# Optimization experiments

Measured on AMD Instinct MI355X. Metric: run time of the kernel, lower is better.

The kernel has to match this reference:

```python
import jax, jax.numpy as jnp
import numpy as np
import math

B, L, LC = 2, 2048, 2048
D_MODEL, D_CROSS, D_HEAD = 1024, 1024, 64
N_HEADS = D_MODEL // D_HEAD
D6 = D_HEAD // 6  # freq bands per spatial axis (k-diffusion AxialRoPE, 3 axes)
EPS = 1e-6


def rope_freqs():
    n = N_HEADS * D6
    f = jnp.exp(jnp.linspace(math.log(math.pi), math.log(10.0 * math.pi), n + 1)[:-1])
    return f.reshape(D6, N_HEADS).T  # [nh, d6]


def rope_theta(pos):
    # pos: [b, l, 3] -> theta: [b, nh, l, 3*d6]
    f = rope_freqs()
    th = jnp.concatenate([pos[..., None, a:a + 1] * f for a in range(3)], axis=-1)  # [b,l,nh,3*d6]
    return jnp.moveaxis(th, -2, -3)


def apply_rotary(x, theta):
    d = theta.shape[-1]
    x1, x2, x3 = x[..., :d], x[..., d:2 * d], x[..., 2 * d:]
    c, s = jnp.cos(theta), jnp.sin(theta)
    return jnp.concatenate([x1 * c - x2 * s, x2 * c + x1 * s, x3], axis=-1)


def rms_norm(x, scale, eps=EPS):
    ms = jnp.mean(x * x, axis=-1, keepdims=True)
    return x * (scale * jax.lax.rsqrt(ms + eps))


def cosine_scale(q, k, scale, eps=EPS):
    s = jnp.sqrt(scale)[:, None, None]  # [nh,1,1]
    qn = q * (s * jax.lax.rsqrt(jnp.sum(q * q, axis=-1, keepdims=True) + eps))
    kn = k * (s * jax.lax.rsqrt(jnp.sum(k * k, axis=-1, keepdims=True) + eps))
    return qn, kn


def setup_inputs():
    key = jax.random.key(0)
    ks = jax.random.split(key, 8)
    return {
        "x": jax.random.normal(ks[0], (B, L, D_MODEL), jnp.float32),
        "pos": jax.random.uniform(ks[1], (B, L, 3), jnp.float32),
        "x_cross": jax.random.normal(ks[2], (B, LC, D_CROSS), jnp.float32),
        "pos_cross": jax.random.uniform(ks[3], (B, LC, 3), jnp.float32),
        "norm_scale": jnp.ones((D_MODEL,), jnp.float32),
        "norm_cross_scale": jnp.ones((D_CROSS,), jnp.float32),
        "q_w": jax.random.normal(ks[4], (D_MODEL, D_MODEL), jnp.float32) * 0.02,
        "kv_w": jax.random.normal(ks[5], (2 * D_MODEL, D_CROSS), jnp.float32) * 0.02,
        "head_scale": jnp.full((N_HEADS,), 10.0, jnp.float32),
        "out_w": jax.random.normal(ks[6], (D_MODEL, D_MODEL), jnp.float32) * 0.02,
    }


def reference(x, pos, x_cross, pos_cross, norm_scale, norm_cross_scale, q_w, kv_w, head_scale, out_w):
    skip = x
    xn = rms_norm(x, norm_scale)
    xc = rms_norm(x_cross, norm_cross_scale)
    q = xn @ q_w.T                       # [b,l,d]
    kv = xc @ kv_w.T                     # [b,lc,2d]
    b, l, _ = q.shape
    lc = kv.shape[1]
    q = q.reshape(b, l, N_HEADS, D_HEAD).transpose(0, 2, 1, 3)          # [b,nh,l,e]
    kv = kv.reshape(b, lc, 2, N_HEADS, D_HEAD)                          # (t nh e) factorization
    k = kv[:, :, 0].transpose(0, 2, 1, 3)
    v = kv[:, :, 1].transpose(0, 2, 1, 3)
    q, k = cosine_scale(q, k, head_scale)
    q = apply_rotary(q, rope_theta(pos))
    k = apply_rotary(k, rope_theta(pos_cross))
    attn = jax.nn.softmax(jnp.einsum('bhqe,bhke->bhqk', q, k), axis=-1)  # scale=1.0 (cosine-sim pre-scaled)
    o = jnp.einsum('bhqk,bhke->bhqe', attn, v)
    o = o.transpose(0, 2, 1, 3).reshape(b, l, D_MODEL)
    return o @ out_w.T + skip
```

## Files before the change

### kernel.cpp

```cpp
#include <hip/hip_runtime.h>

typedef __bf16 bf16_t;
typedef __bf16 bf16x4 __attribute__((ext_vector_type(4)));
typedef __bf16 bf16x8 __attribute__((ext_vector_type(8)));
typedef float f32x4 __attribute__((ext_vector_type(4)));
typedef short s16x4 __attribute__((ext_vector_type(4)));

#define B_DIM 2
#define L_DIM 2048
#define LC_DIM 2048
#define DM 1024
#define NH 16
#define DH 64
#define MB (1u << 20)
#define LOG2E 1.44269504088896f

__device__ __forceinline__ bool probe_is_f32(const unsigned* probe) {
  return probe[0] == 0x3F800000u;
}

__device__ __forceinline__ void async16(const bf16_t* g, bf16_t* l) {
  __builtin_amdgcn_global_load_lds((const __attribute__((address_space(1))) void*)g,
                                   (__attribute__((address_space(3))) void*)l, 16, 0, 0);
}

#if __has_builtin(__builtin_amdgcn_mfma_f32_16x16x16bf16_1k)
#define HAVE_K16 1
__device__ __forceinline__ f32x4 mfma16(bf16x4 a, bf16x4 b, f32x4 c) {
  union { bf16x4 h; s16x4 s; } ua, ub;
  ua.h = a; ub.h = b;
  return __builtin_amdgcn_mfma_f32_16x16x16bf16_1k(ua.s, ub.s, c, 0, 0, 0);
}
#else
#define HAVE_K16 0
#endif

__device__ __forceinline__ void conv_b(const void* src, bf16_t* dst, int i, bool f32) {
  bf16x4 w;
  if (f32) {
    f32x4 v = *(const f32x4*)((const float*)src + i);
    w[0] = (bf16_t)v[0]; w[1] = (bf16_t)v[1]; w[2] = (bf16_t)v[2]; w[3] = (bf16_t)v[3];
  } else {
    w = *(const bf16x4*)((const bf16_t*)src + i);
  }
  *(bf16x4*)(dst + i) = w;
}
__device__ __forceinline__ void conv_f(const void* src, float* dst, int i, int n, bool f32) {
  if (i >= n) return;
  f32x4 v;
  if (f32) {
    v = *(const f32x4*)((const float*)src + i);
  } else {
    bf16x4 w = *(const bf16x4*)((const bf16_t*)src + i);
    v[0] = (float)w[0]; v[1] = (float)w[1]; v[2] = (float)w[2]; v[3] = (float)w[3];
  }
  *(f32x4*)(dst + i) = v;
}

__global__ __launch_bounds__(256) void front_k(
    const void* x, const void* xc, const void* qw, const void* kvw, const void* ow,
    const void* pos, const void* posc, const void* ns, const void* ncs, const void* hs,
    bf16_t* xn, bf16_t* xcn, bf16_t* cqw, bf16_t* ckvw, bf16_t* cow,
    float* fpos, float* fposc, float* fns, float* fncs, float* fhs,
    const unsigned* probe) {
  const bool f32 = probe_is_f32(probe);
  const int tid = threadIdx.x;
  if (blockIdx.x < 2 * B_DIM * L_DIM) {
    const bool isB = blockIdx.x >= B_DIM * L_DIM;
    const int row = isB ? blockIdx.x - B_DIM * L_DIM : blockIdx.x;
    const void* src = isB ? xc : x;
    const void* scr = isB ? ncs : ns;
    bf16_t* out = isB ? xcn : xn;
    float f0, f1, f2, f3, s0, s1, s2, s3;
    if (f32) {
      f32x4 v = *((const f32x4*)((const float*)src + (size_t)row * DM) + tid);
      f0 = v[0]; f1 = v[1]; f2 = v[2]; f3 = v[3];
      f32x4 sv = *((const f32x4*)scr + tid);
      s0 = sv[0]; s1 = sv[1]; s2 = sv[2]; s3 = sv[3];
    } else {
      bf16x4 v = *((const bf16x4*)((const bf16_t*)src + (size_t)row * DM) + tid);
      f0 = (float)v[0]; f1 = (float)v[1]; f2 = (float)v[2]; f3 = (float)v[3];
      bf16x4 sv = *((const bf16x4*)scr + tid);
      s0 = (float)sv[0]; s1 = (float)sv[1]; s2 = (float)sv[2]; s3 = (float)sv[3];
    }
    float ss = f0 * f0 + f1 * f1 + f2 * f2 + f3 * f3;
#pragma unroll
    for (int m = 1; m < 64; m <<= 1) ss += __shfl_xor(ss, m, 64);
    __shared__ float red[4];
    const int wave = tid >> 6, lane = tid & 63;
    if (lane == 0) red[wave] = ss;
    __syncthreads();
    float ms = (red[0] + red[1] + red[2] + red[3]) * (1.0f / DM);
    float r = rsqrtf(ms + 1e-6f);
    bf16x4 w;
    w[0] = (bf16_t)(f0 * r * s0);
    w[1] = (bf16_t)(f1 * r * s1);
    w[2] = (bf16_t)(f2 * r * s2);
    w[3] = (bf16_t)(f3 * r * s3);
    *(bf16x4*)(out + (size_t)row * DM + tid * 4) = w;
    return;
  }
  const int blk = blockIdx.x - 2 * B_DIM * L_DIM;
  const int e4 = tid * 4;
  if (blk < 1024)       conv_b(qw,  cqw,  blk * 1024 + e4, f32);
  else if (blk < 3072)  conv_b(kvw, ckvw, (blk - 1024) * 1024 + e4, f32);
  else if (blk < 4096)  conv_b(ow,  cow,  (blk - 3072) * 1024 + e4, f32);
  else if (blk < 4108)  conv_f(pos,  fpos,  (blk - 4096) * 1024 + e4, 12288, f32);
  else if (blk < 4120)  conv_f(posc, fposc, (blk - 4108) * 1024 + e4, 12288, f32);
  else if (blk == 4120) conv_f(ns,  fns,  e4, 1024, f32);
  else if (blk == 4121) conv_f(ncs, fncs, e4, 1024, f32);
  else                  conv_f(hs,  fhs,  e4, 16, f32);
}

__global__ __launch_bounds__(256) void gemm_qkv_k(const bf16_t* __restrict__ xn,
                                                  const bf16_t* __restrict__ xcn,
                                                  const bf16_t* __restrict__ qw,
                                                  const bf16_t* __restrict__ kvw,
                                                  bf16_t* __restrict__ qb,
                                                  bf16_t* __restrict__ kvK,
                                                  bf16_t* __restrict__ Vp) {
  __shared__ bf16_t Asm[128 * 32];
  __shared__ bf16_t Wsm[128 * 32];
  const int tid = threadIdx.x;
  const int wave = tid >> 6, lane = tid & 63;
  const int quad = lane >> 4, tc = lane & 15;
  const int wr = wave >> 1, wc = wave & 1;
  const bool isq = blockIdx.y < 8;
  const bf16_t* A = isq ? xn : xcn;
  const bf16_t* W = isq ? qw : kvw;
  const int n0 = (isq ? blockIdx.y : (blockIdx.y - 8)) * 128;
  const int m0 = blockIdx.x * 128;
  const int K = 1024;

  const int srow = wave * 16 + (lane >> 2);
  const int scol = (lane & 3) * 8;
  const bf16_t* ag = A + (size_t)(m0 + srow) * K + scol;
  const bf16_t* wg = W + (size_t)(n0 + srow) * K + scol;
  bf16_t* al0 = &Asm[(wave * 16) * 32];
  bf16_t* al1 = &Asm[(64 + wave * 16) * 32];
  bf16_t* wl0 = &Wsm[(wave * 16) * 32];
  bf16_t* wl1 = &Wsm[(64 + wave * 16) * 32];

  f32x4 acc[4][4] = {};

  for (int k0 = 0; k0 < K; k0 += 32) {
    async16(ag + k0, al0);
    async16(ag + k0 + (size_t)64 * K, al1);
    async16(wg + k0, wl0);
    async16(wg + k0 + (size_t)64 * K, wl1);
    __syncthreads();
    bf16x8 af[4], wf[4];
#pragma unroll
    for (int i = 0; i < 4; ++i)
      af[i] = *(const bf16x8*)&Asm[(wr * 64 + i * 16 + tc) * 32 + quad * 8];
#pragma unroll
    for (int j = 0; j < 4; ++j)
      wf[j] = *(const bf16x8*)&Wsm[(wc * 64 + j * 16 + tc) * 32 + quad * 8];
#pragma unroll
    for (int i = 0; i < 4; ++i)
#pragma unroll
      for (int j = 0; j < 4; ++j)
        acc[i][j] = __builtin_amdgcn_mfma_f32_16x16x32_bf16(af[i], wf[j], acc[i][j], 0, 0, 0);
    __syncthreads();
  }

  if (isq || n0 < DM) {
    bf16_t* C = isq ? qb : kvK;
#pragma unroll
    for (int i = 0; i < 4; ++i) {
      const size_t row = (size_t)m0 + wr * 64 + i * 16 + quad * 4;
#pragma unroll
      for (int j = 0; j < 4; ++j) {
        const int col = n0 + wc * 64 + j * 16 + tc;
#pragma unroll
        for (int r = 0; r < 4; ++r)
          C[(row + r) * DM + col] = (bf16_t)acc[i][j][r];
      }
    }
  } else {
#pragma unroll
    for (int i = 0; i < 4; ++i) {
      const int row = m0 + wr * 64 + i * 16 + quad * 4;
      const int b = row >> 11, kc = row & (LC_DIM - 1);
#pragma unroll
      for (int j = 0; j < 4; ++j) {
        const int hd = n0 - DM + wc * 64 + j * 16 + tc;
        const int h = hd >> 6, d = hd & 63;
        bf16x4 pk;
        pk[0] = (bf16_t)acc[i][j][0];
        pk[1] = (bf16_t)acc[i][j][1];
        pk[2] = (bf16_t)acc[i][j][2];
        pk[3] = (bf16_t)acc[i][j][3];
        *(bf16x4*)(Vp + (((size_t)(b * NH + h) * (LC_DIM / 4) + (kc >> 2)) * DH + d) * 4) = pk;
      }
    }
  }
}

__global__ __launch_bounds__(256) void prep_k(bf16_t* __restrict__ q,
                                              const bf16_t* __restrict__ kvK,
                                              bf16_t* __restrict__ Kp,
                                              const float* __restrict__ pos,
                                              const float* __restrict__ pos_cross,
                                              const float* __restrict__ head_scale) {
  const int gw = (blockIdx.x * blockDim.x + threadIdx.x) >> 6;
  const int lane = threadIdx.x & 63;
  const int per = B_DIM * L_DIM * NH;
  const bool is_k = gw >= per;
  const int id = is_k ? gw - per : gw;
  const int h = id & 15;
  const int row = id >> 4;
  const bf16_t* src = (is_k ? kvK : q) + (size_t)row * DM + h * DH;
  const float* pp = (is_k ? pos_cross : pos) + (size_t)row * 3;

  float val = (float)src[lane];
  float ss = val * val;
#pragma unroll
  for (int m = 1; m < 64; m <<= 1) ss += __shfl_xor(ss, m, 64);
  float sc = sqrtf(head_scale[h]) * rsqrtf(ss + 1e-6f);
  if (!is_k) sc *= LOG2E;
  float vn = val * sc;

  const int j = lane;
  const int tj = j < 30 ? j : (j < 60 ? j - 30 : 0);
  const int a = tj >= 20 ? 2 : (tj >= 10 ? 1 : 0);
  const int jj = tj - a * 10;
  float p = pp[a];
  float freq = 3.14159265358979f * expf((float)(jj * 16 + h) * 0.014391156831f);
  float th = p * freq;
  float cth = cosf(th), sth = sinf(th);
  const int partner = j < 30 ? j + 30 : (j < 60 ? j - 30 : j);
  float vp = __shfl(vn, partner, 64);
  float outv;
  if (j < 30)       outv = vn * cth - vp * sth;
  else if (j < 60)  outv = vn * cth + vp * sth;
  else              outv = vn;

  if (is_k) {
    const int b = row >> 11, l = row & (LC_DIM - 1);
    Kp[(((size_t)b * NH + h) * LC_DIM + l) * DH + lane] = (bf16_t)outv;
  } else {
    q[(size_t)row * DM + h * DH + lane] = (bf16_t)outv;
  }
}

__global__ __launch_bounds__(64, 4) void flash6_k(const bf16_t* __restrict__ q,
                                                  const bf16_t* __restrict__ Kp,
                                                  const bf16_t* __restrict__ Vp,
                                                  bf16_t* __restrict__ Op,
                                                  float* __restrict__ lp) {
  const int lane = threadIdx.x;
  const int quad = lane >> 4, tc = lane & 15;
  const int bh = blockIdx.y, b = bh >> 4;
  const int z = blockIdx.z;
  const int q0 = blockIdx.x * 32;

  bf16x8 qf[2][2];
#pragma unroll
  for (int jj = 0; jj < 2; ++jj)
#pragma unroll
    for (int hf = 0; hf < 2; ++hf)
      qf[jj][hf] = *(const bf16x8*)(q + (size_t)(b * L_DIM + q0 + jj * 16 + tc) * DM +
                                    (bh & 15) * DH + hf * 32 + quad * 8);

  f32x4 accO[2][4] = {};
  const bf16_t* kg = Kp + (size_t)bh * LC_DIM * DH;
  const bf16_t* vp = Vp + (size_t)bh * (LC_DIM / 4) * DH * 4;

#if HAVE_K16
  f32x4 accL[2] = {};
  bf16x4 ones;
  ones[0] = (bf16_t)1.0f; ones[1] = (bf16_t)1.0f;
  ones[2] = (bf16_t)1.0f; ones[3] = (bf16_t)1.0f;
#else
  __shared__ bf16_t Psm[32 * 64];
  float lsum[2] = {0.f, 0.f};
  const int sw = tc & 7;
#endif

#pragma unroll 1
  for (int kc0 = z * 1024; kc0 < z * 1024 + 1024; kc0 += 64) {
    bf16x8 kfr[4][2];
#pragma unroll
    for (int mt = 0; mt < 4; ++mt)
#pragma unroll
      for (int hf = 0; hf < 2; ++hf)
        kfr[mt][hf] = *(const bf16x8*)(kg + (size_t)(kc0 + mt * 16 + tc) * DH +
                                       hf * 32 + quad * 8);

#if HAVE_K16
    bf16x4 vf[4][4];
#pragma unroll
    for (int mt = 0; mt < 4; ++mt)
#pragma unroll
      for (int dt = 0; dt < 4; ++dt)
        vf[mt][dt] = *(const bf16x4*)(vp + ((size_t)((kc0 >> 2) + mt * 4 + quad) * DH +
                                            dt * 16 + tc) * 4);

#pragma unroll
    for (int jj = 0; jj < 2; ++jj) {
      f32x4 s[4];
#pragma unroll
      for (int mt = 0; mt < 4; ++mt) {
        f32x4 zf = {0.f, 0.f, 0.f, 0.f};
        zf = __builtin_amdgcn_mfma_f32_16x16x32_bf16(kfr[mt][0], qf[jj][0], zf, 0, 0, 0);
        zf = __builtin_amdgcn_mfma_f32_16x16x32_bf16(kfr[mt][1], qf[jj][1], zf, 0, 0, 0);
        s[mt] = zf;
      }
      bf16x4 p[4];
#pragma unroll
      for (int mt = 0; mt < 4; ++mt) {
        p[mt][0] = (bf16_t)__builtin_amdgcn_exp2f(s[mt][0]);
        p[mt][1] = (bf16_t)__builtin_amdgcn_exp2f(s[mt][1]);
        p[mt][2] = (bf16_t)__builtin_amdgcn_exp2f(s[mt][2]);
        p[mt][3] = (bf16_t)__builtin_amdgcn_exp2f(s[mt][3]);
      }
#pragma unroll
      for (int mt = 0; mt < 4; ++mt) {
        accL[jj] = mfma16(p[mt], ones, accL[jj]);
#pragma unroll
        for (int dt = 0; dt < 4; ++dt)
          accO[jj][dt] = mfma16(p[mt], vf[mt][dt], accO[jj][dt]);
      }
    }
#else
#pragma unroll
    for (int jj = 0; jj < 2; ++jj) {
      f32x4 s[4];
#pragma unroll
      for (int mt = 0; mt < 4; ++mt) {
        f32x4 zf = {0.f, 0.f, 0.f, 0.f};
        zf = __builtin_amdgcn_mfma_f32_16x16x32_bf16(kfr[mt][0], qf[jj][0], zf, 0, 0, 0);
        zf = __builtin_amdgcn_mfma_f32_16x16x32_bf16(kfr[mt][1], qf[jj][1], zf, 0, 0, 0);
        s[mt] = zf;
      }
#pragma unroll
      for (int mt = 0; mt < 4; ++mt) {
        float p0 = __builtin_amdgcn_exp2f(s[mt][0]);
        float p1 = __builtin_amdgcn_exp2f(s[mt][1]);
        float p2 = __builtin_amdgcn_exp2f(s[mt][2]);
        float p3 = __builtin_amdgcn_exp2f(s[mt][3]);
        lsum[jj] += (p0 + p1) + (p2 + p3);
        bf16x4 pk;
        pk[0] = (bf16_t)p0; pk[1] = (bf16_t)p1; pk[2] = (bf16_t)p2; pk[3] = (bf16_t)p3;
        const int phys = (mt * 2 + (quad >> 1)) ^ sw;
        *(bf16x4*)&Psm[(jj * 16 + tc) * 64 + phys * 8 + (quad & 1) * 4] = pk;
      }
    }
#pragma unroll
    for (int kb = 0; kb < 2; ++kb) {
      bf16x8 vfull[4];
#pragma unroll
      for (int dt = 0; dt < 4; ++dt) {
        const size_t k4 = (size_t)((kc0 + kb * 32) >> 2) + quad * 2;
        bf16x4 lo = *(const bf16x4*)(vp + (k4 * DH + dt * 16 + tc) * 4);
        bf16x4 hi = *(const bf16x4*)(vp + ((k4 + 1) * DH + dt * 16 + tc) * 4);
#pragma unroll
        for (int e = 0; e < 4; ++e) { vfull[dt][e] = lo[e]; vfull[dt][4 + e] = hi[e]; }
      }
#pragma unroll
      for (int jp = 0; jp < 2; ++jp) {
        bf16x8 pf = *(const bf16x8*)&Psm[(jp * 16 + tc) * 64 + ((kb * 4 + quad) ^ sw) * 8];
#pragma unroll
        for (int dt = 0; dt < 4; ++dt)
          accO[jp][dt] = __builtin_amdgcn_mfma_f32_16x16x32_bf16(pf, vfull[dt], accO[jp][dt], 0, 0, 0);
      }
    }
#endif
  }

  bf16_t* Ob = Op + (size_t)(z * 32 + bh) * L_DIM * DH;
  float* lb = lp + (size_t)(z * 32 + bh) * L_DIM;
#if HAVE_K16
#pragma unroll
  for (int jj = 0; jj < 2; ++jj) {
    if (tc == 0) {
#pragma unroll
      for (int r = 0; r < 4; ++r) lb[q0 + jj * 16 + quad * 4 + r] = accL[jj][r];
    }
#pragma unroll
    for (int r = 0; r < 4; ++r) {
      const size_t qg = q0 + jj * 16 + quad * 4 + r;
#pragma unroll
      for (int dt = 0; dt < 4; ++dt)
        Ob[qg * DH + dt * 16 + tc] = (bf16_t)accO[jj][dt][r];
    }
  }
#else
#pragma unroll
  for (int jj = 0; jj < 2; ++jj) {
    lsum[jj] += __shfl_xor(lsum[jj], 16, 64);
    lsum[jj] += __shfl_xor(lsum[jj], 32, 64);
  }
#pragma unroll
  for (int jj = 0; jj < 2; ++jj) {
    if (quad == 0) lb[q0 + jj * 16 + tc] = lsum[jj];
#pragma unroll
    for (int r = 0; r < 4; ++r) {
      const size_t qg = q0 + jj * 16 + quad * 4 + r;
#pragma unroll
      for (int dt = 0; dt < 4; ++dt)
        Ob[qg * DH + dt * 16 + tc] = (bf16_t)accO[jj][dt][r];
    }
  }
#endif
}

__global__ __launch_bounds__(256) void combine_k(const bf16_t* __restrict__ Op,
                                                 const float* __restrict__ lp,
                                                 bf16_t* __restrict__ ob) {
  const size_t t = (size_t)blockIdx.x * 256 + threadIdx.x;
  const int bh = (int)(t >> 15);
  const int rem = (int)(t & 32767);
  const int l = rem >> 4, d4 = (rem & 15) * 4;
  const size_t base = ((size_t)bh * L_DIM + l) * DH + d4;
  const size_t zoff = (size_t)32 * L_DIM * DH;
  bf16x4 a0 = *(const bf16x4*)(Op + base);
  bf16x4 a1 = *(const bf16x4*)(Op + zoff + base);
  const float linv = 1.f / (lp[(size_t)bh * L_DIM + l] + lp[(size_t)32 * L_DIM + bh * L_DIM + l]);
  bf16x4 w;
#pragma unroll
  for (int e = 0; e < 4; ++e) w[e] = (bf16_t)(((float)a0[e] + (float)a1[e]) * linv);
  const int b = bh >> 4, h = bh & 15;
  *(bf16x4*)(ob + ((size_t)(b * L_DIM + l)) * DM + h * DH + d4) = w;
}

__global__ __launch_bounds__(256) void gemm_out_k(const bf16_t* __restrict__ A,
                                                  const bf16_t* __restrict__ W,
                                                  const void* __restrict__ skip_raw,
                                                  void* __restrict__ out,
                                                  const unsigned* __restrict__ probe) {
  __shared__ bf16_t Asm[64 * 32];
  __shared__ bf16_t Wsm[128 * 32];
  const int tid = threadIdx.x;
  const int wave = tid >> 6, lane = tid & 63;
  const int quad = lane >> 4, tc = lane & 15;
  const int wr = wave >> 1, wc = wave & 1;
  const int m0 = blockIdx.x * 64, n0 = blockIdx.y * 128;
  const int K = 1024, N = 1024;

  const int srow = wave * 16 + (lane >> 2);
  const int scol = (lane & 3) * 8;
  const bf16_t* ag = A + (size_t)(m0 + srow) * K + scol;
  const bf16_t* wg = W + (size_t)(n0 + srow) * K + scol;
  bf16_t* al = &Asm[(wave * 16) * 32];
  bf16_t* wl0 = &Wsm[(wave * 16) * 32];
  bf16_t* wl1 = &Wsm[(64 + wave * 16) * 32];

  f32x4 acc[2][4] = {};

  for (int k0 = 0; k0 < K; k0 += 32) {
    async16(ag + k0, al);
    async16(wg + k0, wl0);
    async16(wg + k0 + (size_t)64 * K, wl1);
    __syncthreads();
    bf16x8 af[2], wf[4];
#pragma unroll
    for (int i = 0; i < 2; ++i)
      af[i] = *(const bf16x8*)&Asm[(wr * 32 + i * 16 + tc) * 32 + quad * 8];
#pragma unroll
    for (int j = 0; j < 4; ++j)
      wf[j] = *(const bf16x8*)&Wsm[(wc * 64 + j * 16 + tc) * 32 + quad * 8];
#pragma unroll
    for (int i = 0; i < 2; ++i)
#pragma unroll
      for (int j = 0; j < 4; ++j)
        acc[i][j] = __builtin_amdgcn_mfma_f32_16x16x32_bf16(af[i], wf[j], acc[i][j], 0, 0, 0);
    __syncthreads();
  }

  const bool f32o = probe_is_f32(probe);
#pragma unroll
  for (int i = 0; i < 2; ++i) {
    const size_t row = (size_t)m0 + wr * 32 + i * 16 + quad * 4;
#pragma unroll
    for (int j = 0; j < 4; ++j) {
      const int col = n0 + wc * 64 + j * 16 + tc;
#pragma unroll
      for (int r = 0; r < 4; ++r) {
        const size_t idx = (row + r) * (size_t)N + col;
        float v = acc[i][j][r];
        if (f32o) {
          v += ((const float*)skip_raw)[idx];
          ((float*)out)[idx] = v;
        } else {
          v += (float)((const bf16_t*)skip_raw)[idx];
          ((bf16_t*)out)[idx] = (bf16_t)v;
        }
      }
    }
  }
}

extern "C" void kernel_launch(void* const* d_in, const int* in_sizes, int n_in,
                              void* d_out, int out_size, void* d_ws, size_t ws_size,
                              hipStream_t stream) {
  const unsigned* probe = (const unsigned*)d_in[4];
  char* ws = (char*)d_ws;

  bf16_t* cow  = (bf16_t*)(ws + 0 * MB);
  bf16_t* cqw  = (bf16_t*)(ws + 2 * MB);
  bf16_t* ckvw = (bf16_t*)(ws + 4 * MB);
  bf16_t* xn   = (bf16_t*)(ws + 8 * MB);
  bf16_t* xcn  = (bf16_t*)(ws + 16 * MB);
  bf16_t* Op   = (bf16_t*)(ws + 8 * MB);
  bf16_t* kvK  = (bf16_t*)(ws + 24 * MB);
  bf16_t* qb   = (bf16_t*)(ws + 32 * MB);
  bf16_t* Vp   = (bf16_t*)(ws + 40 * MB);
  bf16_t* Kp   = (bf16_t*)(ws + 48 * MB);
  bf16_t* ob   = (bf16_t*)(ws + 56 * MB);
  float* lp    = (float*)(ws + 64 * MB);
  float* fpos  = (float*)(ws + 65 * MB);
  float* fposc = (float*)(ws + 65 * MB + 64 * 1024);
  float* fns   = (float*)(ws + 65 * MB + 128 * 1024);
  float* fncs  = (float*)(ws + 65 * MB + 144 * 1024);
  float* fhs   = (float*)(ws + 65 * MB + 160 * 1024);

  front_k<<<2 * B_DIM * L_DIM + 4123, 256, 0, stream>>>(
      d_in[0], d_in[2], d_in[6], d_in[7], d_in[9], d_in[1], d_in[3], d_in[4],
      d_in[5], d_in[8], xn, xcn, cqw, ckvw, cow, fpos, fposc, fns, fncs, fhs, probe);
  gemm_qkv_k<<<dim3(32, 24), 256, 0, stream>>>(xn, xcn, cqw, ckvw, qb, kvK, Vp);
  prep_k<<<(2 * B_DIM * L_DIM * NH) / 4, 256, 0, stream>>>(qb, kvK, Kp, fpos, fposc, fhs);
  flash6_k<<<dim3(L_DIM / 32, B_DIM * NH, 2), 64, 0, stream>>>(qb, Kp, Vp, Op, lp);
  combine_k<<<4096, 256, 0, stream>>>(Op, lp, ob);
  gemm_out_k<<<dim3(64, 8), 256, 0, stream>>>(ob, cow, d_in[0], d_out, probe);
}
```

Before: 293.1 us.

## Double-buffer K/V register loads and double query rows per flash wave

The flash attention kernel now gives each 64-thread block 64 query rows instead of 32. This halves the number of blocks and doubles how often each loaded K/V tile is reused. In the MFMA path, K and V fragments are software-pipelined with two register buffers, so the next 64-key tile loads while the current one is being computed. The cost is much higher register pressure, with launch bounds lowered to 2 blocks per CU, and less parallelism across the grid.

```diff
diff --git a/kernel.cpp b/kernel.cpp
--- a/kernel.cpp
+++ b/kernel.cpp
@@ -244,7 +244,44 @@
   }
 }
 
-__global__ __launch_bounds__(64, 4) void flash6_k(const bf16_t* __restrict__ q,
+#define FLASH_LOAD(KB, VB, KC)                                                   \
+  {                                                                              \
+    _Pragma("unroll") for (int mt = 0; mt < 4; ++mt) {                           \
+      _Pragma("unroll") for (int hf = 0; hf < 2; ++hf)                           \
+        KB[mt][hf] = *(const bf16x8*)(kg + (size_t)((KC) + mt * 16 + tc) * DH +  \
+                                      hf * 32 + quad * 8);                       \
+      _Pragma("unroll") for (int dt = 0; dt < 4; ++dt)                           \
+        VB[mt][dt] = *(const bf16x4*)(vp + ((size_t)(((KC) >> 2) + mt * 4 + quad) * DH + \
+                                            dt * 16 + tc) * 4);                  \
+    }                                                                            \
+  }
+
+#define FLASH_COMPUTE(KB, VB)                                                    \
+  {                                                                              \
+    _Pragma("unroll") for (int jj = 0; jj < 4; ++jj) {                           \
+      f32x4 s[4];                                                                \
+      _Pragma("unroll") for (int mt = 0; mt < 4; ++mt) {                         \
+        f32x4 zf = {0.f, 0.f, 0.f, 0.f};                                         \
+        zf = __builtin_amdgcn_mfma_f32_16x16x32_bf16(KB[mt][0], qf[jj][0], zf, 0, 0, 0); \
+        zf = __builtin_amdgcn_mfma_f32_16x16x32_bf16(KB[mt][1], qf[jj][1], zf, 0, 0, 0); \
+        s[mt] = zf;                                                              \
+      }                                                                          \
+      bf16x4 p[4];                                                               \
+      _Pragma("unroll") for (int mt = 0; mt < 4; ++mt) {                         \
+        p[mt][0] = (bf16_t)__builtin_amdgcn_exp2f(s[mt][0]);                     \
+        p[mt][1] = (bf16_t)__builtin_amdgcn_exp2f(s[mt][1]);                     \
+        p[mt][2] = (bf16_t)__builtin_amdgcn_exp2f(s[mt][2]);                     \
+        p[mt][3] = (bf16_t)__builtin_amdgcn_exp2f(s[mt][3]);                     \
+      }                                                                          \
+      _Pragma("unroll") for (int mt = 0; mt < 4; ++mt) {                         \
+        accL[jj] = mfma16(p[mt], ones, accL[jj]);                                \
+        _Pragma("unroll") for (int dt = 0; dt < 4; ++dt)                         \
+          accO[jj][dt] = mfma16(p[mt], VB[mt][dt], accO[jj][dt]);                \
+      }                                                                          \
+    }                                                                            \
+  }
+
+__global__ __launch_bounds__(64, 2) void flash7_k(const bf16_t* __restrict__ q,
                                                   const bf16_t* __restrict__ Kp,
                                                   const bf16_t* __restrict__ Vp,
                                                   bf16_t* __restrict__ Op,
@@ -253,33 +290,43 @@
   const int quad = lane >> 4, tc = lane & 15;
   const int bh = blockIdx.y, b = bh >> 4;
   const int z = blockIdx.z;
-  const int q0 = blockIdx.x * 32;
-
-  bf16x8 qf[2][2];
-#pragma unroll
-  for (int jj = 0; jj < 2; ++jj)
+  const int q0 = blockIdx.x * 64;
+
+  bf16x8 qf[4][2];
+#pragma unroll
+  for (int jj = 0; jj < 4; ++jj)
 #pragma unroll
     for (int hf = 0; hf < 2; ++hf)
       qf[jj][hf] = *(const bf16x8*)(q + (size_t)(b * L_DIM + q0 + jj * 16 + tc) * DM +
                                     (bh & 15) * DH + hf * 32 + quad * 8);
 
-  f32x4 accO[2][4] = {};
+  f32x4 accO[4][4] = {};
   const bf16_t* kg = Kp + (size_t)bh * LC_DIM * DH;
   const bf16_t* vp = Vp + (size_t)bh * (LC_DIM / 4) * DH * 4;
+  const int base = z * 1024;
 
 #if HAVE_K16
-  f32x4 accL[2] = {};
+  f32x4 accL[4] = {};
   bf16x4 ones;
   ones[0] = (bf16_t)1.0f; ones[1] = (bf16_t)1.0f;
   ones[2] = (bf16_t)1.0f; ones[3] = (bf16_t)1.0f;
+
+  bf16x8 k0f[4][2], k1f[4][2];
+  bf16x4 v0f[4][4], v1f[4][4];
+  FLASH_LOAD(k0f, v0f, base);
+#pragma unroll 1
+  for (int kc0 = base; kc0 < base + 1024; kc0 += 128) {
+    FLASH_LOAD(k1f, v1f, kc0 + 64);
+    FLASH_COMPUTE(k0f, v0f);
+    if (kc0 + 128 < base + 1024) FLASH_LOAD(k0f, v0f, kc0 + 128);
+    FLASH_COMPUTE(k1f, v1f);
+  }
 #else
-  __shared__ bf16_t Psm[32 * 64];
-  float lsum[2] = {0.f, 0.f};
+  __shared__ bf16_t Psm[64 * 64];
+  float lsum[4] = {0.f, 0.f, 0.f, 0.f};
   const int sw = tc & 7;
-#endif
-
 #pragma unroll 1
-  for (int kc0 = z * 1024; kc0 < z * 1024 + 1024; kc0 += 64) {
+  for (int kc0 = base; kc0 < base + 1024; kc0 += 64) {
     bf16x8 kfr[4][2];
 #pragma unroll
     for (int mt = 0; mt < 4; ++mt)
@@ -287,45 +334,8 @@
       for (int hf = 0; hf < 2; ++hf)
         kfr[mt][hf] = *(const bf16x8*)(kg + (size_t)(kc0 + mt * 16 + tc) * DH +
                                        hf * 32 + quad * 8);
-
-#if HAVE_K16
-    bf16x4 vf[4][4];
-#pragma unroll
-    for (int mt = 0; mt < 4; ++mt)
-#pragma unroll
-      for (int dt = 0; dt < 4; ++dt)
-        vf[mt][dt] = *(const bf16x4*)(vp + ((size_t)((kc0 >> 2) + mt * 4 + quad) * DH +
-                                            dt * 16 + tc) * 4);
-
-#pragma unroll
-    for (int jj = 0; jj < 2; ++jj) {
-      f32x4 s[4];
-#pragma unroll
-      for (int mt = 0; mt < 4; ++mt) {
-        f32x4 zf = {0.f, 0.f, 0.f, 0.f};
-        zf = __builtin_amdgcn_mfma_f32_16x16x32_bf16(kfr[mt][0], qf[jj][0], zf, 0, 0, 0);
-        zf = __builtin_amdgcn_mfma_f32_16x16x32_bf16(kfr[mt][1], qf[jj][1], zf, 0, 0, 0);
-        s[mt] = zf;
-      }
-      bf16x4 p[4];
-#pragma unroll
-      for (int mt = 0; mt < 4; ++mt) {
-        p[mt][0] = (bf16_t)__builtin_amdgcn_exp2f(s[mt][0]);
-        p[mt][1] = (bf16_t)__builtin_amdgcn_exp2f(s[mt][1]);
-        p[mt][2] = (bf16_t)__builtin_amdgcn_exp2f(s[mt][2]);
-        p[mt][3] = (bf16_t)__builtin_amdgcn_exp2f(s[mt][3]);
-      }
-#pragma unroll
-      for (int mt = 0; mt < 4; ++mt) {
-        accL[jj] = mfma16(p[mt], ones, accL[jj]);
-#pragma unroll
-        for (int dt = 0; dt < 4; ++dt)
-          accO[jj][dt] = mfma16(p[mt], vf[mt][dt], accO[jj][dt]);
-      }
-    }
-#else
-#pragma unroll
-    for (int jj = 0; jj < 2; ++jj) {
+#pragma unroll
+    for (int jj = 0; jj < 4; ++jj) {
       f32x4 s[4];
 #pragma unroll
       for (int mt = 0; mt < 4; ++mt) {
@@ -359,21 +369,21 @@
         for (int e = 0; e < 4; ++e) { vfull[dt][e] = lo[e]; vfull[dt][4 + e] = hi[e]; }
       }
 #pragma unroll
-      for (int jp = 0; jp < 2; ++jp) {
+      for (int jp = 0; jp < 4; ++jp) {
         bf16x8 pf = *(const bf16x8*)&Psm[(jp * 16 + tc) * 64 + ((kb * 4 + quad) ^ sw) * 8];
 #pragma unroll
         for (int dt = 0; dt < 4; ++dt)
           accO[jp][dt] = __builtin_amdgcn_mfma_f32_16x16x32_bf16(pf, vfull[dt], accO[jp][dt], 0, 0, 0);
       }
     }
+  }
 #endif
-  }
 
   bf16_t* Ob = Op + (size_t)(z * 32 + bh) * L_DIM * DH;
   float* lb = lp + (size_t)(z * 32 + bh) * L_DIM;
 #if HAVE_K16
 #pragma unroll
-  for (int jj = 0; jj < 2; ++jj) {
+  for (int jj = 0; jj < 4; ++jj) {
     if (tc == 0) {
 #pragma unroll
       for (int r = 0; r < 4; ++r) lb[q0 + jj * 16 + quad * 4 + r] = accL[jj][r];
@@ -388,12 +398,12 @@
   }
 #else
 #pragma unroll
-  for (int jj = 0; jj < 2; ++jj) {
+  for (int jj = 0; jj < 4; ++jj) {
     lsum[jj] += __shfl_xor(lsum[jj], 16, 64);
     lsum[jj] += __shfl_xor(lsum[jj], 32, 64);
   }
 #pragma unroll
-  for (int jj = 0; jj < 2; ++jj) {
+  for (int jj = 0; jj < 4; ++jj) {
     if (quad == 0) lb[q0 + jj * 16 + tc] = lsum[jj];
 #pragma unroll
     for (int r = 0; r < 4; ++r) {
@@ -521,7 +531,7 @@
       d_in[5], d_in[8], xn, xcn, cqw, ckvw, cow, fpos, fposc, fns, fncs, fhs, probe);
   gemm_qkv_k<<<dim3(32, 24), 256, 0, stream>>>(xn, xcn, cqw, ckvw, qb, kvK, Vp);
   prep_k<<<(2 * B_DIM * L_DIM * NH) / 4, 256, 0, stream>>>(qb, kvK, Kp, fpos, fposc, fhs);
-  flash6_k<<<dim3(L_DIM / 32, B_DIM * NH, 2), 64, 0, stream>>>(qb, Kp, Vp, Op, lp);
+  flash7_k<<<dim3(L_DIM / 64, B_DIM * NH, 2), 64, 0, stream>>>(qb, Kp, Vp, Op, lp);
   combine_k<<<4096, 256, 0, stream>>>(Op, lp, ob);
   gemm_out_k<<<dim3(64, 8), 256, 0, stream>>>(ob, cow, d_in[0], d_out, probe);
 }
```

Result: faster. 266.8 us (-9.0%).
